# Optimization experiments

Hardware: AMD Instinct MI355X
Metric: run time of the kernel (lower is better)

The kernel has to match this reference:

```python
import jax, jax.numpy as jnp
import numpy as np


def squash(x, axis=-1):
    # norm_sq/(1+norm_sq) * x/norm, exactly as the torch version
    norm_sq = jnp.sum(x * x, axis=axis, keepdims=True)
    norm = jnp.sqrt(norm_sq)
    return norm_sq / (1.0 + norm_sq) * (x / norm)


def setup_inputs() -> dict:
    key = jax.random.key(0)
    k1, k2 = jax.random.split(key)
    batch, in_caps, in_hid, out_caps, out_hid = 128, 1152, 16, 32, 16
    input_capsules = jax.random.normal(k1, (batch, in_caps, in_hid), dtype=jnp.float32)
    # EinMix weight: 'in_caps in_hid out_caps out_hid'
    W = jax.random.normal(k2, (in_caps, in_hid, out_caps, out_hid), dtype=jnp.float32) * 0.05
    return {"input_capsules": input_capsules, "W": W, "routing_iterations": 3}


def reference(input_capsules, W, routing_iterations):
    # U: [batch, in_caps, out_caps, out_hid]
    U = jnp.einsum('bih,ihoj->bioj', input_capsules, W)
    batch, in_caps, out_caps, out_hid = U.shape
    B = jnp.zeros((batch, in_caps, out_caps), dtype=U.dtype)
    V = None
    for _ in range(routing_iterations):
        C = jax.nn.softmax(B, axis=-1)           # [b, i, o]
        S = jnp.einsum('bio,bioh->boh', C, U)    # [b, o, h]
        V = squash(S, axis=-1)                   # [b, o, h]
        B = B + jnp.einsum('bioh,boh->bio', U, V)
    return V
```

## Files before the change

### kernel.cpp

```cpp
#include <hip/hip_runtime.h>
#include <hip/hip_bf16.h>


#define IN_CAPS 1152
#define OUT_CAPS 32
#define BATCH 128
#define IPC 18
#define NBLK_I (IN_CAPS / IPC)
#define SV_ELEMS (BATCH * OUT_CAPS * 16)

typedef __attribute__((ext_vector_type(8))) short short8;
typedef __attribute__((ext_vector_type(4))) float f32x4;

__device__ inline unsigned f2bf(float x) {
  unsigned u = __builtin_bit_cast(unsigned, x);
  return (u + 0x7FFFu + ((u >> 16) & 1u)) >> 16;
}

__global__ __launch_bounds__(256) void conv_w(const float* __restrict__ W,
                                              unsigned short* __restrict__ Wb) {
  __shared__ float st[16 * 516];
  const int t = threadIdx.x;
  const size_t ibase = (size_t)blockIdx.x * 8192;
  const float4* src = (const float4*)(W + ibase);
#pragma unroll
  for (int r = 0; r < 8; ++r) {
    const int f = r * 256 + t;
    const int k = f >> 7, c4 = f & 127;
    *(float4*)&st[k * 516 + c4 * 4] = src[f];
  }
  __syncthreads();
  unsigned short* dst = Wb + ibase;
#pragma unroll
  for (int r = 0; r < 4; ++r) {
    const int u = r * 256 + t;
    const int o = u >> 5, l = u & 31;
    const int col = o * 16 + (l & 15), k0 = (l >> 4) * 8;
    unsigned b[8];
#pragma unroll
    for (int j = 0; j < 8; ++j) b[j] = f2bf(st[(k0 + j) * 516 + col]);
    uint4 outv;
    outv.x = b[0] | (b[1] << 16);
    outv.y = b[2] | (b[3] << 16);
    outv.z = b[4] | (b[5] << 16);
    outv.w = b[6] | (b[7] << 16);
    *(uint4*)(dst + (size_t)u * 8) = outv;
  }
}

__device__ __forceinline__ void build_xs(const float* __restrict__ X, int bg,
                                         int i0, int t, unsigned (*xs)[64][4]) {
#pragma unroll
  for (int rep = 0; rep < IPC * 256 / 512; ++rep) {
    const int base = rep * 512 + t;
    const int ii = base >> 8;
    const int e = base & 255;
    const int l2 = e >> 2, ju = e & 3;
    unsigned val = 0;
    if (l2 < 32) {
      const float2 f = *(const float2*)(X +
          ((size_t)(bg * 16 + (l2 & 15)) * IN_CAPS + (i0 + ii)) * 16 +
          (l2 >> 4) * 8 + 2 * ju);
      val = f2bf(f.x) | (f2bf(f.y) << 16);
    }
    xs[ii][l2][ju] = val;
  }
}

__device__ __forceinline__ short8 ld_x(const unsigned (*xs)[64][4], int ii, int l) {
  return __builtin_bit_cast(short8, *(const uint4*)(&xs[ii][l][0]));
}

__global__ __launch_bounds__(512, 4)
void caps_pass1(const unsigned short* __restrict__ Wb,
                const float* __restrict__ X, float* __restrict__ P) {
  __shared__ __align__(16) unsigned xs[IPC][64][4];
  const int t = threadIdx.x, w = t >> 6, l = t & 63;
  const int q = l >> 4, bl = l & 15;
  const int gx = blockIdx.x, iblk = gx & 63, bg = gx >> 6;
  const int i0 = iblk * IPC;

  build_xs(X, bg, i0, t, xs);
  __syncthreads();

  const short8* wp = (const short8*)Wb + ((size_t)i0 * 32 + w * 4) * 32 + (l & 31);
  f32x4 sacc[4];
#pragma unroll
  for (int m = 0; m < 4; ++m) sacc[m] = (f32x4){0.f, 0.f, 0.f, 0.f};

  for (int ii = 0; ii < IPC; ++ii) {
    short8 x = ld_x(xs, ii, l);
    short8 a0 = wp[0], a1 = wp[32], a2 = wp[64], a3 = wp[96];
    wp += 1024;
    sacc[0] = __builtin_amdgcn_mfma_f32_16x16x32_bf16(a0, x, sacc[0], 0, 0, 0);
    sacc[1] = __builtin_amdgcn_mfma_f32_16x16x32_bf16(a1, x, sacc[1], 0, 0, 0);
    sacc[2] = __builtin_amdgcn_mfma_f32_16x16x32_bf16(a2, x, sacc[2], 0, 0, 0);
    sacc[3] = __builtin_amdgcn_mfma_f32_16x16x32_bf16(a3, x, sacc[3], 0, 0, 0);
  }
  float* pp = P + ((size_t)iblk * 128 + bg * 16 + bl) * 512 + w * 64 + q * 4;
#pragma unroll
  for (int m = 0; m < 4; ++m) *(f32x4*)(pp + m * 16) = sacc[m] * (1.f / 32.f);
}

__global__ __launch_bounds__(512, 4)
void caps_pass23(const unsigned short* __restrict__ Wb,
                 const float* __restrict__ X,
                 const float* __restrict__ Vt,
                 float* __restrict__ P) {
  __shared__ __align__(16) unsigned xs[IPC][64][4];
  __shared__ float part[4][8][16];
  const int t = threadIdx.x, w = t >> 6, l = t & 63;
  const int q = l >> 4, bl = l & 15;
  const int gx = blockIdx.x, iblk = gx & 63, bg = gx >> 6;
  const int i0 = iblk * IPC;

  f32x4 v[4], sacc[4];
#pragma unroll
  for (int m = 0; m < 4; ++m) {
    v[m] = ((const f32x4*)Vt)[((size_t)(bg * 8 + w) * 64 + l) * 4 + m];
    sacc[m] = (f32x4){0.f, 0.f, 0.f, 0.f};
  }

  build_xs(X, bg, i0, t, xs);
  __syncthreads();

  const short8* wp = (const short8*)Wb + ((size_t)i0 * 32 + w * 4) * 32 + (l & 31);
  short8 an[4];
  short8 xn = ld_x(xs, 0, l);
#pragma unroll
  for (int m = 0; m < 4; ++m) an[m] = wp[m * 32];
  wp += 1024;

  for (int pr2 = 0; pr2 < IPC / 2; ++pr2) {
    f32x4 dk0[4], dk1[4];
    const int s0 = (pr2 & 1) * 2;
    {
      short8 ac[4];
      short8 xc = xn;
#pragma unroll
      for (int m = 0; m < 4; ++m) ac[m] = an[m];
      xn = ld_x(xs, 2 * pr2 + 1, l);
#pragma unroll
      for (int m = 0; m < 4; ++m) an[m] = wp[m * 32];
      wp += 1024;
      const f32x4 z = {0.f, 0.f, 0.f, 0.f};
      f32x4 d[4];
      float e[4];
#pragma unroll
      for (int m = 0; m < 4; ++m)
        d[m] = __builtin_amdgcn_mfma_f32_16x16x32_bf16(ac[m], xc, z, 0, 0, 0);
#pragma unroll
      for (int m = 0; m < 4; ++m) {
        f32x4 pm = d[m] * v[m];
        float p = (pm[0] + pm[1]) + (pm[2] + pm[3]);
        p += __shfl_xor(p, 16);
        p += __shfl_xor(p, 32);
        e[m] = __expf(p);
      }
      if (q == 0) part[s0][w][bl] = (e[0] + e[1]) + (e[2] + e[3]);
#pragma unroll
      for (int m = 0; m < 4; ++m) dk0[m] = d[m] * e[m];
    }
    {
      const int ii = 2 * pr2 + 1;
      short8 ac[4];
      short8 xc = xn;
#pragma unroll
      for (int m = 0; m < 4; ++m) ac[m] = an[m];
      if (ii + 1 < IPC) {
        xn = ld_x(xs, ii + 1, l);
#pragma unroll
        for (int m = 0; m < 4; ++m) an[m] = wp[m * 32];
        wp += 1024;
      }
      const f32x4 z = {0.f, 0.f, 0.f, 0.f};
      f32x4 d[4];
      float e[4];
#pragma unroll
      for (int m = 0; m < 4; ++m)
        d[m] = __builtin_amdgcn_mfma_f32_16x16x32_bf16(ac[m], xc, z, 0, 0, 0);
#pragma unroll
      for (int m = 0; m < 4; ++m) {
        f32x4 pm = d[m] * v[m];
        float p = (pm[0] + pm[1]) + (pm[2] + pm[3]);
        p += __shfl_xor(p, 16);
        p += __shfl_xor(p, 32);
        e[m] = __expf(p);
      }
      if (q == 0) part[s0 + 1][w][bl] = (e[0] + e[1]) + (e[2] + e[3]);
#pragma unroll
      for (int m = 0; m < 4; ++m) dk1[m] = d[m] * e[m];
    }
    __syncthreads();
    float den0 = 0.f, den1 = 0.f;
#pragma unroll
    for (int ww = 0; ww < 8; ++ww) {
      den0 += part[s0][ww][bl];
      den1 += part[s0 + 1][ww][bl];
    }
    const float r0 = __builtin_amdgcn_rcpf(den0);
    const float r1 = __builtin_amdgcn_rcpf(den1);
#pragma unroll
    for (int m = 0; m < 4; ++m) sacc[m] += dk0[m] * r0 + dk1[m] * r1;
  }

  float* pp = P + ((size_t)iblk * 128 + bg * 16 + bl) * 512 + w * 64 + q * 4;
#pragma unroll
  for (int m = 0; m < 4; ++m) *(f32x4*)(pp + m * 16) = sacc[m];
}

template <int MODE>
__global__ __launch_bounds__(256)
void reduce_squash(const float* __restrict__ P, float* __restrict__ Vt,
                   float* __restrict__ V1p, float* __restrict__ Out) {
  __shared__ f32x4 red[8][32];
  const int t = threadIdx.x, qd = t & 31, kq = t >> 5;
  const int j4 = blockIdx.x * 32 + qd;
  const f32x4* p = (const f32x4*)P + j4 + (size_t)kq * 8 * (SV_ELEMS / 4);
  f32x4 s = {0.f, 0.f, 0.f, 0.f};
#pragma unroll
  for (int k = 0; k < 8; ++k) s += p[(size_t)k * (SV_ELEMS / 4)];
  red[kq][qd] = s;
  __syncthreads();
  if (t < 32) {
    f32x4 a = red[0][t];
#pragma unroll
    for (int k2 = 1; k2 < 8; ++k2) a += red[k2][t];
    float ns = a[0] * a[0] + a[1] * a[1] + a[2] * a[2] + a[3] * a[3];
    ns += __shfl_xor(ns, 1);
    ns += __shfl_xor(ns, 2);
    const float sc = ns / ((1.f + ns) * sqrtf(ns));
    f32x4 vv = a * sc;
    if constexpr (MODE == 2) {
      ((f32x4*)Out)[j4] = vv;
    } else {
      if constexpr (MODE == 0) ((f32x4*)V1p)[j4] = vv;
      if constexpr (MODE == 1) vv += ((const f32x4*)V1p)[j4];
#pragma unroll
      for (int c = 0; c < 4; ++c) {
        const int j = j4 * 4 + c;
        const int b = j >> 9, oh = j & 511, o = oh >> 4, h = oh & 15;
        const int bg = b >> 4, bl = b & 15, w = o >> 2, m = o & 3, qq = h >> 2;
        Vt[(((size_t)(bg * 8 + w) * 64 + qq * 16 + bl) * 16) + m * 4 + (h & 3)] =
            vv[c];
      }
    }
  }
}

extern "C" void kernel_launch(void* const* d_in, const int* in_sizes, int n_in,
                              void* d_out, int out_size, void* d_ws, size_t ws_size,
                              hipStream_t stream) {
  const float* X  = (const float*)d_in[0];
  const float* Wg = (const float*)d_in[1];

  float* P   = (float*)d_ws;
  float* Vt  = P + (size_t)NBLK_I * SV_ELEMS;
  float* V1p = Vt + SV_ELEMS;
  unsigned short* Wb = (unsigned short*)(V1p + SV_ELEMS);
  float* out = (float*)d_out;

  conv_w<<<IN_CAPS, 256, 0, stream>>>(Wg, Wb);

  caps_pass1<<<512, 512, 0, stream>>>(Wb, X, P);
  reduce_squash<0><<<512, 256, 0, stream>>>(P, Vt, V1p, nullptr);

  caps_pass23<<<512, 512, 0, stream>>>(Wb, X, Vt, P);
  reduce_squash<1><<<512, 256, 0, stream>>>(P, Vt, V1p, nullptr);

  caps_pass23<<<512, 512, 0, stream>>>(Wb, X, Vt, P);
  reduce_squash<2><<<512, 256, 0, stream>>>(P, nullptr, nullptr, out);
}
```

Measured before the change: 161.4 us.

## Fuse all routing stages into one cooperative persistent kernel with grid barriers

```diff
diff --git a/kernel.cpp b/kernel.cpp
--- a/kernel.cpp
+++ b/kernel.cpp
@@ -8,6 +8,7 @@
 #define IPC 18
 #define NBLK_I (IN_CAPS / IPC)
 #define SV_ELEMS (BATCH * OUT_CAPS * 16)
+#define GRID 512
 
 typedef __attribute__((ext_vector_type(8))) short short8;
 typedef __attribute__((ext_vector_type(4))) float f32x4;
@@ -17,25 +18,39 @@
   return (u + 0x7FFFu + ((u >> 16) & 1u)) >> 16;
 }
 
-__global__ __launch_bounds__(256) void conv_w(const float* __restrict__ W,
-                                              unsigned short* __restrict__ Wb) {
-  __shared__ float st[16 * 516];
-  const int t = threadIdx.x;
-  const size_t ibase = (size_t)blockIdx.x * 8192;
-  const float4* src = (const float4*)(W + ibase);
-#pragma unroll
-  for (int r = 0; r < 8; ++r) {
-    const int f = r * 256 + t;
+__device__ __forceinline__ void grid_bar(unsigned* __restrict__ ctr,
+                                         unsigned target, int t) {
+  __syncthreads();
+  if (t == 0) {
+    __hip_atomic_fetch_add(ctr, 1u, __ATOMIC_ACQ_REL, __HIP_MEMORY_SCOPE_AGENT);
+    while (__hip_atomic_load(ctr, __ATOMIC_RELAXED, __HIP_MEMORY_SCOPE_AGENT) <
+           target)
+      __builtin_amdgcn_s_sleep(1);
+    __threadfence();
+  }
+  __syncthreads();
+}
+
+__device__ __forceinline__ void conv_i(const float* __restrict__ W,
+                                       unsigned short* __restrict__ Wb,
+                                       float* st, int i, int t) {
+  const float4* src = (const float4*)(W + (size_t)i * 8192);
+  float4 g[4];
+#pragma unroll
+  for (int r = 0; r < 4; ++r) g[r] = src[r * 512 + t];
+#pragma unroll
+  for (int r = 0; r < 4; ++r) {
+    const int f = r * 512 + t;
     const int k = f >> 7, c4 = f & 127;
-    *(float4*)&st[k * 516 + c4 * 4] = src[f];
-  }
-  __syncthreads();
-  unsigned short* dst = Wb + ibase;
-#pragma unroll
-  for (int r = 0; r < 4; ++r) {
-    const int u = r * 256 + t;
-    const int o = u >> 5, l = u & 31;
-    const int col = o * 16 + (l & 15), k0 = (l >> 4) * 8;
+    *(float4*)&st[k * 516 + c4 * 4] = g[r];
+  }
+  __syncthreads();
+  unsigned short* dst = Wb + (size_t)i * 8192;
+#pragma unroll
+  for (int r = 0; r < 2; ++r) {
+    const int uu = r * 512 + t;
+    const int o = uu >> 5, ll = uu & 31;
+    const int col = o * 16 + (ll & 15), k0 = (ll >> 4) * 8;
     unsigned b[8];
 #pragma unroll
     for (int j = 0; j < 8; ++j) b[j] = f2bf(st[(k0 + j) * 516 + col]);
@@ -44,8 +59,9 @@
     outv.y = b[2] | (b[3] << 16);
     outv.z = b[4] | (b[5] << 16);
     outv.w = b[6] | (b[7] << 16);
-    *(uint4*)(dst + (size_t)u * 8) = outv;
-  }
+    *(uint4*)(dst + (size_t)uu * 8) = outv;
+  }
+  __syncthreads();
 }
 
 __device__ __forceinline__ void build_xs(const float* __restrict__ X, int bg,
@@ -71,6 +87,232 @@
   return __builtin_bit_cast(short8, *(const uint4*)(&xs[ii][l][0]));
 }
 
+__device__ __forceinline__ void pass1_phase(const short8* __restrict__ wpb,
+                                            const unsigned (*xs)[64][4],
+                                            float* __restrict__ pp, int l) {
+  const short8* wp = wpb;
+  f32x4 sacc[4];
+#pragma unroll
+  for (int m = 0; m < 4; ++m) sacc[m] = (f32x4){0.f, 0.f, 0.f, 0.f};
+  for (int ii = 0; ii < IPC; ++ii) {
+    short8 x = ld_x(xs, ii, l);
+    short8 a0 = wp[0], a1 = wp[32], a2 = wp[64], a3 = wp[96];
+    wp += 1024;
+    sacc[0] = __builtin_amdgcn_mfma_f32_16x16x32_bf16(a0, x, sacc[0], 0, 0, 0);
+    sacc[1] = __builtin_amdgcn_mfma_f32_16x16x32_bf16(a1, x, sacc[1], 0, 0, 0);
+    sacc[2] = __builtin_amdgcn_mfma_f32_16x16x32_bf16(a2, x, sacc[2], 0, 0, 0);
+    sacc[3] = __builtin_amdgcn_mfma_f32_16x16x32_bf16(a3, x, sacc[3], 0, 0, 0);
+  }
+#pragma unroll
+  for (int m = 0; m < 4; ++m) *(f32x4*)(pp + m * 16) = sacc[m] * (1.f / 32.f);
+}
+
+__device__ __forceinline__ void pass23_phase(const short8* __restrict__ wpb,
+                                             const unsigned (*xs)[64][4],
+                                             float (*part)[8][16],
+                                             const float* __restrict__ Vt,
+                                             float* __restrict__ pp,
+                                             int bg, int w, int l, int q, int bl) {
+  f32x4 v[4], sacc[4];
+#pragma unroll
+  for (int m = 0; m < 4; ++m) {
+    v[m] = ((const f32x4*)Vt)[((size_t)(bg * 8 + w) * 64 + l) * 4 + m];
+    sacc[m] = (f32x4){0.f, 0.f, 0.f, 0.f};
+  }
+
+  const short8* wp = wpb;
+  short8 an[4];
+  short8 xn = ld_x(xs, 0, l);
+#pragma unroll
+  for (int m = 0; m < 4; ++m) an[m] = wp[m * 32];
+  wp += 1024;
+
+  for (int pr2 = 0; pr2 < IPC / 2; ++pr2) {
+    f32x4 dk0[4], dk1[4];
+    const int s0 = (pr2 & 1) * 2;
+    {
+      short8 ac[4];
+      short8 xc = xn;
+#pragma unroll
+      for (int m = 0; m < 4; ++m) ac[m] = an[m];
+      xn = ld_x(xs, 2 * pr2 + 1, l);
+#pragma unroll
+      for (int m = 0; m < 4; ++m) an[m] = wp[m * 32];
+      wp += 1024;
+      const f32x4 z = {0.f, 0.f, 0.f, 0.f};
+      f32x4 d[4];
+      float e[4];
+#pragma unroll
+      for (int m = 0; m < 4; ++m)
+        d[m] = __builtin_amdgcn_mfma_f32_16x16x32_bf16(ac[m], xc, z, 0, 0, 0);
+#pragma unroll
+      for (int m = 0; m < 4; ++m) {
+        f32x4 pm = d[m] * v[m];
+        float p = (pm[0] + pm[1]) + (pm[2] + pm[3]);
+        p += __shfl_xor(p, 16);
+        p += __shfl_xor(p, 32);
+        e[m] = __expf(p);
+      }
+      if (q == 0) part[s0][w][bl] = (e[0] + e[1]) + (e[2] + e[3]);
+#pragma unroll
+      for (int m = 0; m < 4; ++m) dk0[m] = d[m] * e[m];
+    }
+    {
+      const int ii = 2 * pr2 + 1;
+      short8 ac[4];
+      short8 xc = xn;
+#pragma unroll
+      for (int m = 0; m < 4; ++m) ac[m] = an[m];
+      if (ii + 1 < IPC) {
+        xn = ld_x(xs, ii + 1, l);
+#pragma unroll
+        for (int m = 0; m < 4; ++m) an[m] = wp[m * 32];
+        wp += 1024;
+      }
+      const f32x4 z = {0.f, 0.f, 0.f, 0.f};
+      f32x4 d[4];
+      float e[4];
+#pragma unroll
+      for (int m = 0; m < 4; ++m)
+        d[m] = __builtin_amdgcn_mfma_f32_16x16x32_bf16(ac[m], xc, z, 0, 0, 0);
+#pragma unroll
+      for (int m = 0; m < 4; ++m) {
+        f32x4 pm = d[m] * v[m];
+        float p = (pm[0] + pm[1]) + (pm[2] + pm[3]);
+        p += __shfl_xor(p, 16);
+        p += __shfl_xor(p, 32);
+        e[m] = __expf(p);
+      }
+      if (q == 0) part[s0 + 1][w][bl] = (e[0] + e[1]) + (e[2] + e[3]);
+#pragma unroll
+      for (int m = 0; m < 4; ++m) dk1[m] = d[m] * e[m];
+    }
+    __syncthreads();
+    float den0 = 0.f, den1 = 0.f;
+#pragma unroll
+    for (int ww = 0; ww < 8; ++ww) {
+      den0 += part[s0][ww][bl];
+      den1 += part[s0 + 1][ww][bl];
+    }
+    const float r0 = __builtin_amdgcn_rcpf(den0);
+    const float r1 = __builtin_amdgcn_rcpf(den1);
+#pragma unroll
+    for (int m = 0; m < 4; ++m) sacc[m] += dk0[m] * r0 + dk1[m] * r1;
+  }
+
+#pragma unroll
+  for (int m = 0; m < 4; ++m) *(f32x4*)(pp + m * 16) = sacc[m];
+}
+
+template <int MODE>
+__device__ __forceinline__ void reduce_phase(const float* __restrict__ P,
+                                             float* __restrict__ Vt,
+                                             float* __restrict__ V1p,
+                                             float* __restrict__ Out,
+                                             int bid, int t, f32x4 (*red)[32]) {
+  const int qd = t & 31, kq = t >> 5;
+  const int j4 = bid * 32 + qd;
+  const f32x4* p = (const f32x4*)P + j4 + (size_t)kq * 4 * (SV_ELEMS / 4);
+  f32x4 s = {0.f, 0.f, 0.f, 0.f};
+#pragma unroll
+  for (int k = 0; k < 4; ++k) s += p[(size_t)k * (SV_ELEMS / 4)];
+  red[kq][qd] = s;
+  __syncthreads();
+  if (t < 32) {
+    f32x4 a = red[0][t];
+#pragma unroll
+    for (int k2 = 1; k2 < 16; ++k2) a += red[k2][t];
+    float ns = a[0] * a[0] + a[1] * a[1] + a[2] * a[2] + a[3] * a[3];
+    ns += __shfl_xor(ns, 1);
+    ns += __shfl_xor(ns, 2);
+    const float sc = ns / ((1.f + ns) * sqrtf(ns));
+    f32x4 vv = a * sc;
+    if constexpr (MODE == 2) {
+      ((f32x4*)Out)[j4] = vv;
+    } else {
+      if constexpr (MODE == 0) ((f32x4*)V1p)[j4] = vv;
+      if constexpr (MODE == 1) vv += ((const f32x4*)V1p)[j4];
+#pragma unroll
+      for (int c = 0; c < 4; ++c) {
+        const int j = j4 * 4 + c;
+        const int b = j >> 9, oh = j & 511, o = oh >> 4, h = oh & 15;
+        const int bg = b >> 4, bl = b & 15, w = o >> 2, m = o & 3, qq = h >> 2;
+        Vt[(((size_t)(bg * 8 + w) * 64 + qq * 16 + bl) * 16) + m * 4 + (h & 3)] =
+            vv[c];
+      }
+    }
+  }
+  __syncthreads();
+}
+
+__global__ __launch_bounds__(512, 4)
+void caps_one(const float* __restrict__ W, const float* __restrict__ X,
+              unsigned short* __restrict__ Wb, float* __restrict__ P,
+              float* __restrict__ Vt, float* __restrict__ V1p,
+              float* __restrict__ Out, unsigned* __restrict__ ctr) {
+  __shared__ __align__(16) char smem[16 * 516 * 4];
+  float* st = (float*)smem;
+  unsigned (*xs)[64][4] = (unsigned (*)[64][4])smem;
+  float (*part)[8][16] = (float (*)[8][16])(smem + 18432);
+  f32x4 (*red)[32] = (f32x4(*)[32])(smem + 18432 + 2048);
+
+  const int t = threadIdx.x, w = t >> 6, l = t & 63;
+  const int q = l >> 4, bl = l & 15;
+  const int bid = blockIdx.x, iblk = bid & 63, sub = bid >> 6, bg = sub;
+  const int i0 = iblk * IPC;
+
+  for (int ii = sub; ii < IPC; ii += 8) conv_i(W, Wb, st, i0 + ii, t);
+
+  build_xs(X, bg, i0, t, xs);
+
+  const short8* wpb = (const short8*)Wb + ((size_t)i0 * 32 + w * 4) * 32 + (l & 31);
+  float* pp = P + ((size_t)iblk * 128 + bg * 16 + bl) * 512 + w * 64 + q * 4;
+
+  grid_bar(ctr, GRID * 1, t);
+  pass1_phase(wpb, xs, pp, l);
+  grid_bar(ctr, GRID * 2, t);
+  reduce_phase<0>(P, Vt, V1p, nullptr, bid, t, red);
+  grid_bar(ctr, GRID * 3, t);
+  pass23_phase(wpb, xs, part, Vt, pp, bg, w, l, q, bl);
+  grid_bar(ctr, GRID * 4, t);
+  reduce_phase<1>(P, Vt, V1p, nullptr, bid, t, red);
+  grid_bar(ctr, GRID * 5, t);
+  pass23_phase(wpb, xs, part, Vt, pp, bg, w, l, q, bl);
+  grid_bar(ctr, GRID * 6, t);
+  reduce_phase<2>(P, nullptr, nullptr, Out, bid, t, red);
+}
+
+__global__ __launch_bounds__(256) void conv_w(const float* __restrict__ W,
+                                              unsigned short* __restrict__ Wb) {
+  __shared__ float st[16 * 516];
+  const int t = threadIdx.x;
+  const size_t ibase = (size_t)blockIdx.x * 8192;
+  const float4* src = (const float4*)(W + ibase);
+#pragma unroll
+  for (int r = 0; r < 8; ++r) {
+    const int f = r * 256 + t;
+    const int k = f >> 7, c4 = f & 127;
+    *(float4*)&st[k * 516 + c4 * 4] = src[f];
+  }
+  __syncthreads();
+  unsigned short* dst = Wb + ibase;
+#pragma unroll
+  for (int r = 0; r < 4; ++r) {
+    const int u = r * 256 + t;
+    const int o = u >> 5, l = u & 31;
+    const int col = o * 16 + (l & 15), k0 = (l >> 4) * 8;
+    unsigned b[8];
+#pragma unroll
+    for (int j = 0; j < 8; ++j) b[j] = f2bf(st[(k0 + j) * 516 + col]);
+    uint4 outv;
+    outv.x = b[0] | (b[1] << 16);
+    outv.y = b[2] | (b[3] << 16);
+    outv.z = b[4] | (b[5] << 16);
+    outv.w = b[6] | (b[7] << 16);
+    *(uint4*)(dst + (size_t)u * 8) = outv;
+  }
+}
+
 __global__ __launch_bounds__(512, 4)
 void caps_pass1(const unsigned short* __restrict__ Wb,
                 const float* __restrict__ X, float* __restrict__ P) {
@@ -79,134 +321,28 @@
   const int q = l >> 4, bl = l & 15;
   const int gx = blockIdx.x, iblk = gx & 63, bg = gx >> 6;
   const int i0 = iblk * IPC;
-
   build_xs(X, bg, i0, t, xs);
   __syncthreads();
-
-  const short8* wp = (const short8*)Wb + ((size_t)i0 * 32 + w * 4) * 32 + (l & 31);
-  f32x4 sacc[4];
-#pragma unroll
-  for (int m = 0; m < 4; ++m) sacc[m] = (f32x4){0.f, 0.f, 0.f, 0.f};
-
-  for (int ii = 0; ii < IPC; ++ii) {
-    short8 x = ld_x(xs, ii, l);
-    short8 a0 = wp[0], a1 = wp[32], a2 = wp[64], a3 = wp[96];
-    wp += 1024;
-    sacc[0] = __builtin_amdgcn_mfma_f32_16x16x32_bf16(a0, x, sacc[0], 0, 0, 0);
-    sacc[1] = __builtin_amdgcn_mfma_f32_16x16x32_bf16(a1, x, sacc[1], 0, 0, 0);
-    sacc[2] = __builtin_amdgcn_mfma_f32_16x16x32_bf16(a2, x, sacc[2], 0, 0, 0);
-    sacc[3] = __builtin_amdgcn_mfma_f32_16x16x32_bf16(a3, x, sacc[3], 0, 0, 0);
-  }
+  const short8* wpb = (const short8*)Wb + ((size_t)i0 * 32 + w * 4) * 32 + (l & 31);
   float* pp = P + ((size_t)iblk * 128 + bg * 16 + bl) * 512 + w * 64 + q * 4;
-#pragma unroll
-  for (int m = 0; m < 4; ++m) *(f32x4*)(pp + m * 16) = sacc[m] * (1.f / 32.f);
+  pass1_phase(wpb, xs, pp, l);
 }
 
 __global__ __launch_bounds__(512, 4)
 void caps_pass23(const unsigned short* __restrict__ Wb,
                  const float* __restrict__ X,
-                 const float* __restrict__ Vt,
-                 float* __restrict__ P) {
+                 const float* __restrict__ Vt, float* __restrict__ P) {
   __shared__ __align__(16) unsigned xs[IPC][64][4];
   __shared__ float part[4][8][16];
   const int t = threadIdx.x, w = t >> 6, l = t & 63;
   const int q = l >> 4, bl = l & 15;
   const int gx = blockIdx.x, iblk = gx & 63, bg = gx >> 6;
   const int i0 = iblk * IPC;
-
-  f32x4 v[4], sacc[4];
-#pragma unroll
-  for (int m = 0; m < 4; ++m) {
-    v[m] = ((const f32x4*)Vt)[((size_t)(bg * 8 + w) * 64 + l) * 4 + m];
-    sacc[m] = (f32x4){0.f, 0.f, 0.f, 0.f};
-  }
-
   build_xs(X, bg, i0, t, xs);
   __syncthreads();
-
-  const short8* wp = (const short8*)Wb + ((size_t)i0 * 32 + w * 4) * 32 + (l & 31);
-  short8 an[4];
-  short8 xn = ld_x(xs, 0, l);
-#pragma unroll
-  for (int m = 0; m < 4; ++m) an[m] = wp[m * 32];
-  wp += 1024;
-
-  for (int pr2 = 0; pr2 < IPC / 2; ++pr2) {
-    f32x4 dk0[4], dk1[4];
-    const int s0 = (pr2 & 1) * 2;
-    {
-      short8 ac[4];
-      short8 xc = xn;
-#pragma unroll
-      for (int m = 0; m < 4; ++m) ac[m] = an[m];
-      xn = ld_x(xs, 2 * pr2 + 1, l);
-#pragma unroll
-      for (int m = 0; m < 4; ++m) an[m] = wp[m * 32];
-      wp += 1024;
-      const f32x4 z = {0.f, 0.f, 0.f, 0.f};
-      f32x4 d[4];
-      float e[4];
-#pragma unroll
-      for (int m = 0; m < 4; ++m)
-        d[m] = __builtin_amdgcn_mfma_f32_16x16x32_bf16(ac[m], xc, z, 0, 0, 0);
-#pragma unroll
-      for (int m = 0; m < 4; ++m) {
-        f32x4 pm = d[m] * v[m];
-        float p = (pm[0] + pm[1]) + (pm[2] + pm[3]);
-        p += __shfl_xor(p, 16);
-        p += __shfl_xor(p, 32);
-        e[m] = __expf(p);
-      }
-      if (q == 0) part[s0][w][bl] = (e[0] + e[1]) + (e[2] + e[3]);
-#pragma unroll
-      for (int m = 0; m < 4; ++m) dk0[m] = d[m] * e[m];
-    }
-    {
-      const int ii = 2 * pr2 + 1;
-      short8 ac[4];
-      short8 xc = xn;
-#pragma unroll
-      for (int m = 0; m < 4; ++m) ac[m] = an[m];
-      if (ii + 1 < IPC) {
-        xn = ld_x(xs, ii + 1, l);
-#pragma unroll
-        for (int m = 0; m < 4; ++m) an[m] = wp[m * 32];
-        wp += 1024;
-      }
-      const f32x4 z = {0.f, 0.f, 0.f, 0.f};
-      f32x4 d[4];
-      float e[4];
-#pragma unroll
-      for (int m = 0; m < 4; ++m)
-        d[m] = __builtin_amdgcn_mfma_f32_16x16x32_bf16(ac[m], xc, z, 0, 0, 0);
-#pragma unroll
-      for (int m = 0; m < 4; ++m) {
-        f32x4 pm = d[m] * v[m];
-        float p = (pm[0] + pm[1]) + (pm[2] + pm[3]);
-        p += __shfl_xor(p, 16);
-        p += __shfl_xor(p, 32);
-        e[m] = __expf(p);
-      }
-      if (q == 0) part[s0 + 1][w][bl] = (e[0] + e[1]) + (e[2] + e[3]);
-#pragma unroll
-      for (int m = 0; m < 4; ++m) dk1[m] = d[m] * e[m];
-    }
-    __syncthreads();
-    float den0 = 0.f, den1 = 0.f;
-#pragma unroll
-    for (int ww = 0; ww < 8; ++ww) {
-      den0 += part[s0][ww][bl];
-      den1 += part[s0 + 1][ww][bl];
-    }
-    const float r0 = __builtin_amdgcn_rcpf(den0);
-    const float r1 = __builtin_amdgcn_rcpf(den1);
-#pragma unroll
-    for (int m = 0; m < 4; ++m) sacc[m] += dk0[m] * r0 + dk1[m] * r1;
-  }
-
+  const short8* wpb = (const short8*)Wb + ((size_t)i0 * 32 + w * 4) * 32 + (l & 31);
   float* pp = P + ((size_t)iblk * 128 + bg * 16 + bl) * 512 + w * 64 + q * 4;
-#pragma unroll
-  for (int m = 0; m < 4; ++m) *(f32x4*)(pp + m * 16) = sacc[m];
+  pass23_phase(wpb, xs, part, Vt, pp, bg, w, l, q, bl);
 }
 
 template <int MODE>
@@ -258,16 +394,23 @@
   float* Vt  = P + (size_t)NBLK_I * SV_ELEMS;
   float* V1p = Vt + SV_ELEMS;
   unsigned short* Wb = (unsigned short*)(V1p + SV_ELEMS);
+  unsigned* ctr = (unsigned*)(Wb + (size_t)IN_CAPS * 8192);
   float* out = (float*)d_out;
 
-  conv_w<<<IN_CAPS, 256, 0, stream>>>(Wg, Wb);
-
-  caps_pass1<<<512, 512, 0, stream>>>(Wb, X, P);
-  reduce_squash<0><<<512, 256, 0, stream>>>(P, Vt, V1p, nullptr);
-
-  caps_pass23<<<512, 512, 0, stream>>>(Wb, X, Vt, P);
-  reduce_squash<1><<<512, 256, 0, stream>>>(P, Vt, V1p, nullptr);
-
-  caps_pass23<<<512, 512, 0, stream>>>(Wb, X, Vt, P);
-  reduce_squash<2><<<512, 256, 0, stream>>>(P, nullptr, nullptr, out);
-}
+  hipMemsetAsync(ctr, 0, 64, stream);
+
+  void* args[] = {(void*)&Wg, (void*)&X, (void*)&Wb, (void*)&P,
+                  (void*)&Vt, (void*)&V1p, (void*)&out, (void*)&ctr};
+  hipError_t err = hipLaunchCooperativeKernel((void*)caps_one, dim3(GRID),
+                                              dim3(512), args, 0, stream);
+  if (err != hipSuccess) {
+    (void)hipGetLastError();
+    conv_w<<<IN_CAPS, 256, 0, stream>>>(Wg, Wb);
+    caps_pass1<<<512, 512, 0, stream>>>(Wb, X, P);
+    reduce_squash<0><<<512, 256, 0, stream>>>(P, Vt, V1p, nullptr);
+    caps_pass23<<<512, 512, 0, stream>>>(Wb, X, Vt, P);
+    reduce_squash<1><<<512, 256, 0, stream>>>(P, Vt, V1p, nullptr);
+    caps_pass23<<<512, 512, 0, stream>>>(Wb, X, Vt, P);
+    reduce_squash<2><<<512, 256, 0, stream>>>(P, nullptr, nullptr, out);
+  }
+}
```

Result: slower. 471.2 us (+191.9%).

## Pack two input capsules per MFMA K-slice and use exp2 with pre-scaled V

Applied to the files above, without the earlier changes.

```diff
diff --git a/kernel.cpp b/kernel.cpp
--- a/kernel.cpp
+++ b/kernel.cpp
@@ -6,35 +6,48 @@
 #define OUT_CAPS 32
 #define BATCH 128
 #define IPC 18
+#define PAIRS (IPC / 2)
 #define NBLK_I (IN_CAPS / IPC)
 #define SV_ELEMS (BATCH * OUT_CAPS * 16)
+#define LOG2E 1.4426950408889634f
 
 typedef __attribute__((ext_vector_type(8))) short short8;
 typedef __attribute__((ext_vector_type(4))) float f32x4;
+
+#if __has_builtin(__builtin_amdgcn_exp2f)
+#define EXP2(x) __builtin_amdgcn_exp2f(x)
+#else
+#define EXP2(x) exp2f(x)
+#endif
 
 __device__ inline unsigned f2bf(float x) {
   unsigned u = __builtin_bit_cast(unsigned, x);
   return (u + 0x7FFFu + ((u >> 16) & 1u)) >> 16;
 }
 
+__device__ __forceinline__ float swz16_add(float p) {
+  const int pi = __builtin_bit_cast(int, p);
+  return p + __builtin_bit_cast(float,
+             __builtin_amdgcn_ds_swizzle(pi, 0x401F));
+}
+
 __global__ __launch_bounds__(256) void conv_w(const float* __restrict__ W,
                                               unsigned short* __restrict__ Wb) {
-  __shared__ float st[16 * 516];
+  __shared__ float st[32 * 516];
   const int t = threadIdx.x;
-  const size_t ibase = (size_t)blockIdx.x * 8192;
-  const float4* src = (const float4*)(W + ibase);
-#pragma unroll
-  for (int r = 0; r < 8; ++r) {
+  const float4* src = (const float4*)(W + (size_t)blockIdx.x * 16384);
+#pragma unroll
+  for (int r = 0; r < 16; ++r) {
     const int f = r * 256 + t;
     const int k = f >> 7, c4 = f & 127;
     *(float4*)&st[k * 516 + c4 * 4] = src[f];
   }
   __syncthreads();
-  unsigned short* dst = Wb + ibase;
-#pragma unroll
-  for (int r = 0; r < 4; ++r) {
+  uint4* dst = (uint4*)(Wb + (size_t)blockIdx.x * 16384);
+#pragma unroll
+  for (int r = 0; r < 8; ++r) {
     const int u = r * 256 + t;
-    const int o = u >> 5, l = u & 31;
+    const int o = u >> 6, l = u & 63;
     const int col = o * 16 + (l & 15), k0 = (l >> 4) * 8;
     unsigned b[8];
 #pragma unroll
@@ -44,37 +57,40 @@
     outv.y = b[2] | (b[3] << 16);
     outv.z = b[4] | (b[5] << 16);
     outv.w = b[6] | (b[7] << 16);
-    *(uint4*)(dst + (size_t)u * 8) = outv;
+    dst[u] = outv;
   }
 }
 
 __device__ __forceinline__ void build_xs(const float* __restrict__ X, int bg,
-                                         int i0, int t, unsigned (*xs)[64][4]) {
-#pragma unroll
-  for (int rep = 0; rep < IPC * 256 / 512; ++rep) {
-    const int base = rep * 512 + t;
-    const int ii = base >> 8;
-    const int e = base & 255;
-    const int l2 = e >> 2, ju = e & 3;
-    unsigned val = 0;
-    if (l2 < 32) {
+                                         int i0, int t, unsigned (*xs)[32][4]) {
+#pragma unroll
+  for (int rep = 0; rep < 5; ++rep) {
+    const int idx = rep * 512 + t;
+    if (idx < IPC * 128) {
+      const int ii = idx >> 7;
+      const int e = idx & 127;
+      const int l2 = e >> 2, ju = e & 3;
       const float2 f = *(const float2*)(X +
           ((size_t)(bg * 16 + (l2 & 15)) * IN_CAPS + (i0 + ii)) * 16 +
           (l2 >> 4) * 8 + 2 * ju);
-      val = f2bf(f.x) | (f2bf(f.y) << 16);
-    }
-    xs[ii][l2][ju] = val;
-  }
-}
-
-__device__ __forceinline__ short8 ld_x(const unsigned (*xs)[64][4], int ii, int l) {
-  return __builtin_bit_cast(short8, *(const uint4*)(&xs[ii][l][0]));
+      xs[ii][l2][ju] = f2bf(f.x) | (f2bf(f.y) << 16);
+    }
+  }
+}
+
+__device__ __forceinline__ uint4 ld_x_pair(const unsigned (*xs)[32][4],
+                                           int pr, int l) {
+  return *(const uint4*)(&xs[2 * pr + (l >> 5)][l & 31][0]);
+}
+
+__device__ __forceinline__ short8 u4s8(uint4 v) {
+  return __builtin_bit_cast(short8, v);
 }
 
 __global__ __launch_bounds__(512, 4)
 void caps_pass1(const unsigned short* __restrict__ Wb,
                 const float* __restrict__ X, float* __restrict__ P) {
-  __shared__ __align__(16) unsigned xs[IPC][64][4];
+  __shared__ __align__(16) unsigned xs[IPC][32][4];
   const int t = threadIdx.x, w = t >> 6, l = t & 63;
   const int q = l >> 4, bl = l & 15;
   const int gx = blockIdx.x, iblk = gx & 63, bg = gx >> 6;
@@ -83,15 +99,16 @@
   build_xs(X, bg, i0, t, xs);
   __syncthreads();
 
-  const short8* wp = (const short8*)Wb + ((size_t)i0 * 32 + w * 4) * 32 + (l & 31);
+  const short8* wp = (const short8*)Wb +
+      ((size_t)iblk * PAIRS) * 2048 + w * 256 + l;
   f32x4 sacc[4];
 #pragma unroll
   for (int m = 0; m < 4; ++m) sacc[m] = (f32x4){0.f, 0.f, 0.f, 0.f};
 
-  for (int ii = 0; ii < IPC; ++ii) {
-    short8 x = ld_x(xs, ii, l);
-    short8 a0 = wp[0], a1 = wp[32], a2 = wp[64], a3 = wp[96];
-    wp += 1024;
+  for (int pr = 0; pr < PAIRS; ++pr) {
+    short8 x = u4s8(ld_x_pair(xs, pr, l));
+    short8 a0 = wp[0], a1 = wp[64], a2 = wp[128], a3 = wp[192];
+    wp += 2048;
     sacc[0] = __builtin_amdgcn_mfma_f32_16x16x32_bf16(a0, x, sacc[0], 0, 0, 0);
     sacc[1] = __builtin_amdgcn_mfma_f32_16x16x32_bf16(a1, x, sacc[1], 0, 0, 0);
     sacc[2] = __builtin_amdgcn_mfma_f32_16x16x32_bf16(a2, x, sacc[2], 0, 0, 0);
@@ -107,8 +124,8 @@
                  const float* __restrict__ X,
                  const float* __restrict__ Vt,
                  float* __restrict__ P) {
-  __shared__ __align__(16) unsigned xs[IPC][64][4];
-  __shared__ float part[4][8][16];
+  __shared__ __align__(16) unsigned xs[IPC][32][4];
+  __shared__ float part[4][16][8];
   const int t = threadIdx.x, w = t >> 6, l = t & 63;
   const int q = l >> 4, bl = l & 15;
   const int gx = blockIdx.x, iblk = gx & 63, bg = gx >> 6;
@@ -124,84 +141,78 @@
   build_xs(X, bg, i0, t, xs);
   __syncthreads();
 
-  const short8* wp = (const short8*)Wb + ((size_t)i0 * 32 + w * 4) * 32 + (l & 31);
+  const short8* wp = (const short8*)Wb +
+      ((size_t)iblk * PAIRS) * 2048 + w * 256 + l;
+  const unsigned zm = (l < 32) ? 0xFFFFFFFFu : 0u;
+
   short8 an[4];
-  short8 xn = ld_x(xs, 0, l);
-#pragma unroll
-  for (int m = 0; m < 4; ++m) an[m] = wp[m * 32];
-  wp += 1024;
-
-  for (int pr2 = 0; pr2 < IPC / 2; ++pr2) {
-    f32x4 dk0[4], dk1[4];
-    const int s0 = (pr2 & 1) * 2;
-    {
-      short8 ac[4];
-      short8 xc = xn;
-#pragma unroll
-      for (int m = 0; m < 4; ++m) ac[m] = an[m];
-      xn = ld_x(xs, 2 * pr2 + 1, l);
-#pragma unroll
-      for (int m = 0; m < 4; ++m) an[m] = wp[m * 32];
-      wp += 1024;
-      const f32x4 z = {0.f, 0.f, 0.f, 0.f};
-      f32x4 d[4];
-      float e[4];
-#pragma unroll
-      for (int m = 0; m < 4; ++m)
-        d[m] = __builtin_amdgcn_mfma_f32_16x16x32_bf16(ac[m], xc, z, 0, 0, 0);
-#pragma unroll
-      for (int m = 0; m < 4; ++m) {
-        f32x4 pm = d[m] * v[m];
-        float p = (pm[0] + pm[1]) + (pm[2] + pm[3]);
-        p += __shfl_xor(p, 16);
-        p += __shfl_xor(p, 32);
-        e[m] = __expf(p);
-      }
-      if (q == 0) part[s0][w][bl] = (e[0] + e[1]) + (e[2] + e[3]);
-#pragma unroll
-      for (int m = 0; m < 4; ++m) dk0[m] = d[m] * e[m];
-    }
-    {
-      const int ii = 2 * pr2 + 1;
-      short8 ac[4];
-      short8 xc = xn;
-#pragma unroll
-      for (int m = 0; m < 4; ++m) ac[m] = an[m];
-      if (ii + 1 < IPC) {
-        xn = ld_x(xs, ii + 1, l);
-#pragma unroll
-        for (int m = 0; m < 4; ++m) an[m] = wp[m * 32];
-        wp += 1024;
-      }
-      const f32x4 z = {0.f, 0.f, 0.f, 0.f};
-      f32x4 d[4];
-      float e[4];
-#pragma unroll
-      for (int m = 0; m < 4; ++m)
-        d[m] = __builtin_amdgcn_mfma_f32_16x16x32_bf16(ac[m], xc, z, 0, 0, 0);
-#pragma unroll
-      for (int m = 0; m < 4; ++m) {
-        f32x4 pm = d[m] * v[m];
-        float p = (pm[0] + pm[1]) + (pm[2] + pm[3]);
-        p += __shfl_xor(p, 16);
-        p += __shfl_xor(p, 32);
-        e[m] = __expf(p);
-      }
-      if (q == 0) part[s0 + 1][w][bl] = (e[0] + e[1]) + (e[2] + e[3]);
-#pragma unroll
-      for (int m = 0; m < 4; ++m) dk1[m] = d[m] * e[m];
+  uint4 xn = ld_x_pair(xs, 0, l);
+#pragma unroll
+  for (int m = 0; m < 4; ++m) an[m] = wp[m * 64];
+  wp += 2048;
+
+  for (int pr = 0; pr < PAIRS; ++pr) {
+    short8 ac[4];
+#pragma unroll
+    for (int m = 0; m < 4; ++m) ac[m] = an[m];
+    uint4 xc = xn;
+    if (pr + 1 < PAIRS) {
+      xn = ld_x_pair(xs, pr + 1, l);
+#pragma unroll
+      for (int m = 0; m < 4; ++m) an[m] = wp[m * 64];
+      wp += 2048;
+    }
+    uint4 x0u, x1u;
+    x0u.x = xc.x & zm; x0u.y = xc.y & zm; x0u.z = xc.z & zm; x0u.w = xc.w & zm;
+    x1u.x = xc.x ^ x0u.x; x1u.y = xc.y ^ x0u.y;
+    x1u.z = xc.z ^ x0u.z; x1u.w = xc.w ^ x0u.w;
+    const short8 x0 = u4s8(x0u), x1 = u4s8(x1u);
+
+    const f32x4 z = {0.f, 0.f, 0.f, 0.f};
+    f32x4 d0[4], d1[4];
+#pragma unroll
+    for (int m = 0; m < 4; ++m)
+      d0[m] = __builtin_amdgcn_mfma_f32_16x16x32_bf16(ac[m], x0, z, 0, 0, 0);
+#pragma unroll
+    for (int m = 0; m < 4; ++m)
+      d1[m] = __builtin_amdgcn_mfma_f32_16x16x32_bf16(ac[m], x1, z, 0, 0, 0);
+
+    float e0[4], e1[4];
+#pragma unroll
+    for (int m = 0; m < 4; ++m) {
+      f32x4 pm = d0[m] * v[m];
+      float p = (pm[0] + pm[1]) + (pm[2] + pm[3]);
+      p = swz16_add(p);
+      p += __shfl_xor(p, 32);
+      e0[m] = EXP2(p);
+    }
+#pragma unroll
+    for (int m = 0; m < 4; ++m) {
+      f32x4 pm = d1[m] * v[m];
+      float p = (pm[0] + pm[1]) + (pm[2] + pm[3]);
+      p = swz16_add(p);
+      p += __shfl_xor(p, 32);
+      e1[m] = EXP2(p);
+    }
+    const int s0 = (pr & 1) * 2;
+    if (q == 0) {
+      part[s0][bl][w] = (e0[0] + e0[1]) + (e0[2] + e0[3]);
+      part[s0 + 1][bl][w] = (e1[0] + e1[1]) + (e1[2] + e1[3]);
     }
     __syncthreads();
-    float den0 = 0.f, den1 = 0.f;
-#pragma unroll
-    for (int ww = 0; ww < 8; ++ww) {
-      den0 += part[s0][ww][bl];
-      den1 += part[s0 + 1][ww][bl];
-    }
+    const f32x4* pd0 = (const f32x4*)&part[s0][bl][0];
+    const f32x4* pd1 = (const f32x4*)&part[s0 + 1][bl][0];
+    f32x4 u0 = pd0[0] + pd0[1];
+    f32x4 u1 = pd1[0] + pd1[1];
+    const float den0 = (u0[0] + u0[1]) + (u0[2] + u0[3]);
+    const float den1 = (u1[0] + u1[1]) + (u1[2] + u1[3]);
     const float r0 = __builtin_amdgcn_rcpf(den0);
     const float r1 = __builtin_amdgcn_rcpf(den1);
 #pragma unroll
-    for (int m = 0; m < 4; ++m) sacc[m] += dk0[m] * r0 + dk1[m] * r1;
+    for (int m = 0; m < 4; ++m) {
+      sacc[m] += d0[m] * (e0[m] * r0);
+      sacc[m] += d1[m] * (e1[m] * r1);
+    }
   }
 
   float* pp = P + ((size_t)iblk * 128 + bg * 16 + bl) * 512 + w * 64 + q * 4;
@@ -236,13 +247,14 @@
     } else {
       if constexpr (MODE == 0) ((f32x4*)V1p)[j4] = vv;
       if constexpr (MODE == 1) vv += ((const f32x4*)V1p)[j4];
+      const f32x4 vs = vv * LOG2E;
 #pragma unroll
       for (int c = 0; c < 4; ++c) {
         const int j = j4 * 4 + c;
         const int b = j >> 9, oh = j & 511, o = oh >> 4, h = oh & 15;
         const int bg = b >> 4, bl = b & 15, w = o >> 2, m = o & 3, qq = h >> 2;
         Vt[(((size_t)(bg * 8 + w) * 64 + qq * 16 + bl) * 16) + m * 4 + (h & 3)] =
-            vv[c];
+            vs[c];
       }
     }
   }
@@ -260,7 +272,7 @@
   unsigned short* Wb = (unsigned short*)(V1p + SV_ELEMS);
   float* out = (float*)d_out;
 
-  conv_w<<<IN_CAPS, 256, 0, stream>>>(Wg, Wb);
+  conv_w<<<IN_CAPS / 2, 256, 0, stream>>>(Wg, Wb);
 
   caps_pass1<<<512, 512, 0, stream>>>(Wb, X, P);
   reduce_squash<0><<<512, 256, 0, stream>>>(P, Vt, V1p, nullptr);
```

After: 150.5 us. 1.07x faster.
